# Kernel tuning notes

Measured on AMD Instinct MI355X. Metric: run time of the kernel, lower is better.

## Reference

```python
import jax, jax.numpy as jnp
import numpy as np

B, D, H, Z, E = 2048, 1024, 1024, 256, 64


def setup_inputs() -> dict:
    key = jax.random.key(0)
    ks = jax.random.split(key, 16)
    s = lambda k, shape, std=0.02: jax.random.normal(k, shape, dtype=jnp.float32) * std
    return {
        "x": jax.random.normal(ks[0], (B, D), dtype=jnp.float32),
        "h0": jax.random.normal(ks[1], (B, H), dtype=jnp.float32),
        "c0": jax.random.normal(ks[2], (B, H), dtype=jnp.float32),
        "hhat0": jax.random.normal(ks[3], (B, Z), dtype=jnp.float32),
        "chat0": jax.random.normal(ks[4], (B, Z), dtype=jnp.float32),
        "hweight": s(ks[5], (Z + H + D, 4 * Z)),
        "hbias": jnp.zeros((4 * Z,), jnp.float32),
        "zweight_h": s(ks[6], (Z, 4 * E), 0.01),
        "zweight_x": s(ks[7], (Z, 4 * E), 0.01),
        "zweight_b": s(ks[8], (Z, 4 * E), 0.01),
        "zbias_h": jnp.ones((4 * E,), jnp.float32),
        "zbias_x": jnp.ones((4 * E,), jnp.float32),
        # stacked in gate order (i, g, f, o), matching the torch cat order
        "dweight_h": jnp.full((4, E, H), 0.1 / E, jnp.float32),
        "dweight_x": jnp.full((4, E, H), 0.1 / E, jnp.float32),
        "dweight_b": s(ks[9], (4, E, H), 0.01),
        "weight": s(ks[10], (H + D, 4 * H)),
        "bias": jnp.zeros((4 * H,), jnp.float32),
    }


def reference(x, h0, c0, hhat0, chat0, hweight, hbias,
              zweight_h, zweight_x, zweight_b, zbias_h, zbias_x,
              dweight_h, dweight_x, dweight_b, weight, bias):
    # ---- hyper LSTM cell ----
    hcat = jnp.concatenate([hhat0, h0, x], axis=1)                 # [B, Z+H+D]
    hg = hcat @ hweight + hbias                                    # [B, 4Z]
    i_h, g_h, f_h, o_h = jnp.split(hg, 4, axis=1)
    chat1 = jax.nn.sigmoid(f_h) * chat0 + jax.nn.sigmoid(i_h) * jnp.tanh(g_h)
    hhat1 = jax.nn.sigmoid(o_h) * jnp.tanh(chat1)                  # [B, Z]

    # ---- embeddings z (gate order i, g, f, o) ----
    z_h = (hhat1 @ zweight_h + zbias_h).reshape(-1, 4, E)          # [B,4,E]
    z_x = (hhat1 @ zweight_x + zbias_x).reshape(-1, 4, E)
    z_b = (hhat1 @ zweight_b).reshape(-1, 4, E)

    # ---- per-gate modulation vectors d_y* : [B,4,H] -> [B,4H] ----
    d_yh = jnp.einsum('bge,geh->bgh', z_h, dweight_h).reshape(-1, 4 * H)
    d_yx = jnp.einsum('bge,geh->bgh', z_x, dweight_x).reshape(-1, 4 * H)
    d_yb = jnp.einsum('bge,geh->bgh', z_b, dweight_b).reshape(-1, 4 * H)

    # ---- main LSTM with hypernetwork modulation ----
    gates = jnp.concatenate([h0, x], axis=1) @ weight              # [B, 4H]
    gates = gates * d_yh * d_yx + d_yb + bias
    i_g, g_g, f_g, o_g = jnp.split(gates, 4, axis=1)
    c1 = jax.nn.sigmoid(f_g) * c0 + jax.nn.sigmoid(i_g) * jnp.tanh(g_g)
    h1 = jax.nn.sigmoid(o_g) * jnp.tanh(c1)
    return (h1, c1, hhat1, chat1)
```

## Files before the change

### kernel.cpp

```cpp
#include <hip/hip_runtime.h>
#include <hip/hip_bf16.h>
#include <math.h>


typedef __attribute__((ext_vector_type(8))) short bf16x8;
typedef __attribute__((ext_vector_type(4))) float f32x4;
typedef unsigned short u16;

__device__ __forceinline__ u16 f2b(float f) {
  union { float f; unsigned u; } v; v.f = f;
  unsigned r = v.u + 0x7fffu + ((v.u >> 16) & 1u);
  return (u16)(r >> 16);
}
__device__ __forceinline__ float b2f(u16 b) {
  union { unsigned u; float f; } v; v.u = ((unsigned)b) << 16; return v.f;
}
__device__ __forceinline__ float sigm(float x) {
  return __builtin_amdgcn_rcpf(1.f + __expf(-x));
}
__device__ __forceinline__ float ftanh(float x) {
  float xc = fminf(fmaxf(x, -15.f), 15.f);
  float t = __expf(2.f * xc);
  return (t - 1.f) * __builtin_amdgcn_rcpf(t + 1.f);
}
__device__ __forceinline__ float sel4(float a, float b, float c, float d, int k) {
  return (k & 2) ? ((k & 1) ? d : c) : ((k & 1) ? b : a);
}

#define GLL16(gsrc, ldst)                                                      \
  __builtin_amdgcn_global_load_lds(                                            \
      (const __attribute__((address_space(1))) void*)(gsrc),                   \
      (__attribute__((address_space(3))) void*)(ldst), 16, 0, 0)

__global__ void k_prep(const float* __restrict__ hhat0, const float* __restrict__ h0,
                       const float* __restrict__ x, const float* __restrict__ weight,
                       const float* __restrict__ hweight,
                       const float* __restrict__ zw_h, const float* __restrict__ zw_x,
                       const float* __restrict__ zw_b, const float* __restrict__ dw_h,
                       const float* __restrict__ dw_x, const float* __restrict__ dw_b,
                       u16* __restrict__ hcatb, u16* __restrict__ bt,
                       u16* __restrict__ zwT, u16* __restrict__ dwT) {
  __shared__ float tile[32][66];
  int bid = blockIdx.x;
  const int t = threadIdx.x;
  if (bid < 4608) {
    int i = bid * 256 + t;
    int b = i / 576, c4 = i % 576;
    const float* src;
    if (c4 < 64)       src = hhat0 + (long)b * 256 + c4 * 4;
    else if (c4 < 320) src = h0 + (long)b * 1024 + (c4 - 64) * 4;
    else               src = x + (long)b * 1024 + (c4 - 320) * 4;
    float4 v = *(const float4*)src;
    ushort4 o = {f2b(v.x), f2b(v.y), f2b(v.z), f2b(v.w)};
    *(ushort4*)&hcatb[(long)b * 2304 + c4 * 4] = o;
    return;
  }
  bid -= 4608;
  if (bid < 5760) {
    const int n0 = (bid % 160) * 32, k0 = (bid / 160) * 64;
    if (n0 < 4096 && k0 < 256) return;
    const int isH = (n0 >= 4096);
    const float* src; int C, sc0, sr0;
    if (isH) { src = hweight; C = 1024; sc0 = n0 - 4096; sr0 = k0; }
    else     { src = weight;  C = 4096; sc0 = n0;        sr0 = k0 - 256; }
    #pragma unroll
    for (int p = 0; p < 8; ++p) {
      int c = t & 31, r = (t >> 5) + 8 * p;
      tile[c][r] = src[(long)(sr0 + r) * C + sc0 + c];
    }
    __syncthreads();
    #pragma unroll
    for (int p = 0; p < 2; ++p) {
      int kc = t & 15, cl = (t >> 4) + 16 * p;
      int orow;
      if (isH) { int u = sc0 + cl; orow = 4096 + ((u & 255) << 2) + (u >> 8); }
      else     orow = n0 + cl;
      ushort4 o = {f2b(tile[cl][4 * kc]), f2b(tile[cl][4 * kc + 1]),
                   f2b(tile[cl][4 * kc + 2]), f2b(tile[cl][4 * kc + 3])};
      *(ushort4*)&bt[(long)orow * 2304 + k0 + 4 * kc] = o;
    }
    return;
  }
  bid -= 5760;
  const int zi = bid >> 5, bx = bid & 31;
  const float* src; u16* dst; int R, C;
  if (zi < 3) {
    src = (zi == 0) ? zw_h : (zi == 1) ? zw_x : zw_b;
    dst = zwT + (long)zi * 65536; R = 256; C = 256;
  } else {
    int s = zi - 3, tt = s >> 2, g = s & 3;
    src = ((tt == 0) ? dw_h : (tt == 1) ? dw_x : dw_b) + (long)g * 65536;
    dst = dwT + (long)s * 65536; R = 64; C = 1024;
  }
  const int nct = C / 32;
  const int c0 = (bx % nct) * 32, r0 = (bx / nct) * 64;
  #pragma unroll
  for (int p = 0; p < 8; ++p) {
    int c = t & 31, r = (t >> 5) + 8 * p;
    tile[c][r] = src[(long)(r0 + r) * C + c0 + c];
  }
  __syncthreads();
  #pragma unroll
  for (int p = 0; p < 2; ++p) {
    int kc = t & 15, cl = (t >> 4) + 16 * p;
    ushort4 o = {f2b(tile[cl][4 * kc]), f2b(tile[cl][4 * kc + 1]),
                 f2b(tile[cl][4 * kc + 2]), f2b(tile[cl][4 * kc + 3])};
    *(ushort4*)&dst[(long)(c0 + cl) * R + r0 + 4 * kc] = o;
  }
}

__global__ __launch_bounds__(512, 4)
void k_gemm_main(const u16* __restrict__ A, const u16* __restrict__ Bt,
                 const float* __restrict__ hbias, const float* __restrict__ chat0,
                 u16* __restrict__ grawb, float* __restrict__ chat1,
                 float* __restrict__ hhat1, u16* __restrict__ hhat1b) {
  constexpr int K = 2304, BK = 64;
  __shared__ __align__(16) u16 sA[2][128 * BK];
  __shared__ __align__(16) u16 sB[2][128 * BK];
  const int m0 = blockIdx.y * 128, n0 = blockIdx.x * 128;
  const int kstart = (n0 < 4096) ? 256 : 0;
  const int tid = threadIdx.x, wave = tid >> 6, lane = tid & 63;
  const int quad = lane >> 4, lrow = lane & 15;
  const int wm = (wave >> 2) * 64, wn = (wave & 3) * 32;

  const int la = tid * 16;
  const int rowa = la >> 7, qa = (((la >> 4) & 7) - rowa) & 7;
  const int lb = 8192 + tid * 16;
  const int rowb = lb >> 7, qb = (((lb >> 4) & 7) - rowb) & 7;
  const long aoff0 = ((long)(m0 + rowa) * K + qa * 8) * 2;
  const long aoff1 = ((long)(m0 + rowb) * K + qb * 8) * 2;
  const long boff0 = ((long)(n0 + rowa) * K + qa * 8) * 2;
  const long boff1 = ((long)(n0 + rowb) * K + qb * 8) * 2;

  const f32x4 vz = {0.f, 0.f, 0.f, 0.f};
  f32x4 acc[4][2];
  #pragma unroll
  for (int i = 0; i < 4; ++i)
    #pragma unroll
    for (int j = 0; j < 2; ++j) acc[i][j] = vz;

  auto stage = [&](int d, int k0) {
    const long kb = (long)k0 * 2;
    GLL16((const char*)A + aoff0 + kb, (char*)sA[d] + wave * 1024);
    GLL16((const char*)A + aoff1 + kb, (char*)sA[d] + 8192 + wave * 1024);
    GLL16((const char*)Bt + boff0 + kb, (char*)sB[d] + wave * 1024);
    GLL16((const char*)Bt + boff1 + kb, (char*)sB[d] + 8192 + wave * 1024);
  };

  auto compute = [&](int d) {
    bf16x8 af[4][2], bf[2][2];
    const char* pA = (const char*)sA[d];
    const char* pB = (const char*)sB[d];
    #pragma unroll
    for (int i = 0; i < 4; ++i) {
      int row = wm + i * 16 + lrow;
      const char* base = pA + row * 128;
      af[i][0] = *(const bf16x8*)(base + (((quad + row) & 7) << 4));
      af[i][1] = *(const bf16x8*)(base + (((4 + quad + row) & 7) << 4));
    }
    #pragma unroll
    for (int j = 0; j < 2; ++j) {
      int row = wn + j * 16 + lrow;
      const char* base = pB + row * 128;
      bf[j][0] = *(const bf16x8*)(base + (((quad + row) & 7) << 4));
      bf[j][1] = *(const bf16x8*)(base + (((4 + quad + row) & 7) << 4));
    }
    #pragma unroll
    for (int kk = 0; kk < 2; ++kk)
      #pragma unroll
      for (int i = 0; i < 4; ++i)
        #pragma unroll
        for (int j = 0; j < 2; ++j)
          acc[i][j] = __builtin_amdgcn_mfma_f32_16x16x32_bf16(af[i][kk], bf[j][kk], acc[i][j], 0, 0, 0);
  };

  const int nt = (K - kstart) >> 6;
  stage(0, kstart);
  for (int t = 0; t < nt - 1; ++t) {
    stage((t + 1) & 1, kstart + (t + 1) * BK);
    asm volatile("s_waitcnt vmcnt(4)" ::: "memory");
    __builtin_amdgcn_sched_barrier(0);
    __builtin_amdgcn_s_barrier();
    __builtin_amdgcn_sched_barrier(0);
    compute(t & 1);
    __builtin_amdgcn_s_barrier();
  }
  asm volatile("s_waitcnt vmcnt(0)" ::: "memory");
  __builtin_amdgcn_sched_barrier(0);
  __builtin_amdgcn_s_barrier();
  compute((nt - 1) & 1);

  if (n0 < 4096) {
    #pragma unroll
    for (int i = 0; i < 4; ++i)
      #pragma unroll
      for (int j = 0; j < 2; ++j)
        #pragma unroll
        for (int r = 0; r < 4; ++r) {
          int row = m0 + wm + i * 16 + quad * 4 + r;
          int col = n0 + wn + j * 16 + lrow;
          grawb[(long)row * 4096 + col] = f2b(acc[i][j][r]);
        }
  } else {
    const int ubase = (n0 - 4096) + wn;
    const int q3 = lane & 3;
    #pragma unroll
    for (int i = 0; i < 4; ++i) {
      #pragma unroll
      for (int j = 0; j < 2; ++j) {
        int u = ubase + j * 16 + lrow;
        int g = u & 3, z = u >> 2;
        float hb = hbias[g * 256 + z];
        float v0 = acc[i][j][0] + hb, v1 = acc[i][j][1] + hb;
        float v2 = acc[i][j][2] + hb, v3 = acc[i][j][3] + hb;
        float s0 = sel4(v0, v1, v2, v3, q3);
        float s1 = __shfl_xor(sel4(v0, v1, v2, v3, q3 ^ 1), 1);
        float s2 = __shfl_xor(sel4(v0, v1, v2, v3, q3 ^ 2), 2);
        float s3 = __shfl_xor(sel4(v0, v1, v2, v3, q3 ^ 3), 3);
        float vi = sel4(s0, s1, s2, s3, q3);
        float vg = sel4(s0, s1, s2, s3, q3 ^ 1);
        float vf = sel4(s0, s1, s2, s3, q3 ^ 2);
        float vo = sel4(s0, s1, s2, s3, q3 ^ 3);
        int row = m0 + wm + i * 16 + quad * 4 + q3;
        float cc = sigm(vf) * chat0[(long)row * 256 + z] + sigm(vi) * ftanh(vg);
        float hh = sigm(vo) * ftanh(cc);
        chat1[(long)row * 256 + z] = cc;
        hhat1[(long)row * 256 + z] = hh;
        hhat1b[(long)row * 256 + z] = f2b(hh);
      }
    }
  }
}

__global__ __launch_bounds__(256, 2)
void k_gemm_z(const u16* __restrict__ A, const u16* __restrict__ Bt,
              const float* __restrict__ zbh, const float* __restrict__ zbx,
              u16* __restrict__ zbout) {
  constexpr int K = 256, BK = 32;
  __shared__ __align__(16) u16 sA[64 * BK];
  __shared__ __align__(16) u16 sB[128 * BK];
  const int m0 = blockIdx.y * 64, n0 = blockIdx.x * 128;
  const int tid = threadIdx.x, wave = tid >> 6, lane = tid & 63;
  const int quad = lane >> 4, lrow = lane & 15;
  const int wm = (wave >> 1) * 32, wn = (wave & 1) * 64;

  const int sl = tid * 16;
  const int arow = sl >> 6;
  const int aq = (((sl & 63) >> 4) - (arow >> 1)) & 3;
  const long aoff = ((long)(m0 + arow) * K) * 2 + aq * 16;

  const f32x4 vz = {0.f, 0.f, 0.f, 0.f};
  f32x4 acc[2][4];
  #pragma unroll
  for (int i = 0; i < 2; ++i)
    #pragma unroll
    for (int j = 0; j < 4; ++j) acc[i][j] = vz;

  for (int k0 = 0; k0 < K; k0 += BK) {
    GLL16((const char*)A + aoff + (long)k0 * 2, (char*)sA + wave * 1024);
    #pragma unroll
    for (int c = 0; c < 2; ++c) {
      int l = c * 4096 + sl;
      int row = l >> 6;
      int q = (((l & 63) >> 4) - (row >> 1)) & 3;
      const char* g = (const char*)Bt + ((long)(n0 + row) * K + k0) * 2 + q * 16;
      GLL16(g, (char*)sB + c * 4096 + wave * 1024);
    }
    __syncthreads();
    bf16x8 af[2], bf[4];
    #pragma unroll
    for (int i = 0; i < 2; ++i) {
      int row = wm + i * 16 + lrow;
      af[i] = *(const bf16x8*)((const char*)sA + row * 64 + (((quad + (row >> 1)) & 3) << 4));
    }
    #pragma unroll
    for (int j = 0; j < 4; ++j) {
      int row = wn + j * 16 + lrow;
      bf[j] = *(const bf16x8*)((const char*)sB + row * 64 + (((quad + (row >> 1)) & 3) << 4));
    }
    #pragma unroll
    for (int i = 0; i < 2; ++i)
      #pragma unroll
      for (int j = 0; j < 4; ++j)
        acc[i][j] = __builtin_amdgcn_mfma_f32_16x16x32_bf16(af[i], bf[j], acc[i][j], 0, 0, 0);
    __syncthreads();
  }
  #pragma unroll
  for (int i = 0; i < 2; ++i) {
    #pragma unroll
    for (int j = 0; j < 4; ++j) {
      #pragma unroll
      for (int r = 0; r < 4; ++r) {
        int row = m0 + wm + i * 16 + quad * 4 + r;
        int col = n0 + wn + j * 16 + lrow;
        float v = acc[i][j][r] + ((col < 256) ? zbh[col] : (col < 512) ? zbx[col - 256] : 0.f);
        zbout[(long)row * 768 + col] = f2b(v);
      }
    }
  }
}

__global__ __launch_bounds__(256, 2)
void k_dmod_lstm(const u16* __restrict__ z, const u16* __restrict__ dwT,
                 const u16* __restrict__ grawb, const float* __restrict__ bias,
                 const float* __restrict__ c0, float* __restrict__ h1,
                 float* __restrict__ c1) {
  __shared__ __align__(16) u16 sZ[64 * 192];
  __shared__ __align__(16) u16 sW[3 * 64 * 64];
  __shared__ __align__(16) u16 sG[2][64 * 64];
  const int m0 = blockIdx.y * 64;
  const int hc0 = blockIdx.x * 64;
  const int tid = threadIdx.x, wave = tid >> 6, lane = tid & 63;
  const int quad = lane >> 4, lrow = lane & 15;
  const int wm = (wave >> 1) * 32, wn = (wave & 1) * 32;
  const f32x4 vz4 = {0.f, 0.f, 0.f, 0.f};

  f32x4 pcar[2][2];
  f32x4 ccar[2][2];

  auto stage = [&](int g) {
    #pragma unroll
    for (int c = 0; c < 6; ++c) {
      int l = c * 4096 + tid * 16;
      int ci = l >> 4, row = ci / 24, p = ci - row * 24;
      int q = p + 72 - row; q -= (q / 24) * 24;
      int tt = q >> 3, e16 = q & 7;
      const char* gz = (const char*)z + (long)(m0 + row) * 1536 + tt * 512 + g * 128 + e16 * 16;
      GLL16(gz, (char*)sZ + c * 4096 + wave * 1024);
      int t2 = l >> 13, rw = (l & 8191) >> 7, p2 = (l >> 4) & 7;
      int q2 = (p2 - rw) & 7;
      const char* gw = (const char*)dwT + (long)((t2 * 4 + g) * 1024 + hc0 + rw) * 128 + q2 * 16;
      GLL16(gw, (char*)sW + c * 4096 + wave * 1024);
    }
    #pragma unroll
    for (int c = 0; c < 2; ++c) {
      int l = c * 4096 + tid * 16;
      int row = l >> 7, off = l & 127;
      const char* gg = (const char*)grawb + ((long)(m0 + row) * 4096 + g * 1024 + hc0) * 2 + off;
      GLL16(gg, (char*)sG[g & 1] + c * 4096 + wave * 1024);
    }
  };

  stage(0);
  #pragma unroll
  for (int g = 0; g < 4; ++g) {
    __syncthreads();
    bf16x8 za2[2][3][2], wb2[2][3][2];
    #pragma unroll
    for (int kk = 0; kk < 2; ++kk) {
      #pragma unroll
      for (int t = 0; t < 3; ++t) {
        #pragma unroll
        for (int i = 0; i < 2; ++i) {
          int row = wm + i * 16 + lrow;
          int q0 = t * 8 + kk * 4 + quad;
          int ph = q0 + row; ph -= (ph / 24) * 24;
          za2[kk][t][i] = *(const bf16x8*)((const char*)sZ + row * 384 + ph * 16);
        }
        #pragma unroll
        for (int j = 0; j < 2; ++j) {
          int row = wn + j * 16 + lrow;
          int ph = ((kk * 4 + quad) + row) & 7;
          wb2[kk][t][j] = *(const bf16x8*)((const char*)sW + t * 8192 + row * 128 + ph * 16);
        }
      }
    }
    __syncthreads();
    if (g < 3) stage(g + 1);
    f32x4 aH[2][2], aX[2][2], aB[2][2];
    #pragma unroll
    for (int i = 0; i < 2; ++i)
      #pragma unroll
      for (int j = 0; j < 2; ++j) { aH[i][j] = vz4; aX[i][j] = vz4; aB[i][j] = vz4; }
    #pragma unroll
    for (int kk = 0; kk < 2; ++kk)
      #pragma unroll
      for (int i = 0; i < 2; ++i)
        #pragma unroll
        for (int j = 0; j < 2; ++j) {
          aH[i][j] = __builtin_amdgcn_mfma_f32_16x16x32_bf16(za2[kk][0][i], wb2[kk][0][j], aH[i][j], 0, 0, 0);
          aX[i][j] = __builtin_amdgcn_mfma_f32_16x16x32_bf16(za2[kk][1][i], wb2[kk][1][j], aX[i][j], 0, 0, 0);
          aB[i][j] = __builtin_amdgcn_mfma_f32_16x16x32_bf16(za2[kk][2][i], wb2[kk][2][j], aB[i][j], 0, 0, 0);
        }
    const u16* sGc = sG[g & 1];
    #pragma unroll
    for (int i = 0; i < 2; ++i) {
      #pragma unroll
      for (int j = 0; j < 2; ++j) {
        #pragma unroll
        for (int r = 0; r < 4; ++r) {
          int rowl = wm + i * 16 + quad * 4 + r;
          int col = wn + j * 16 + lrow;
          int row = m0 + rowl;
          float gr = b2f(sGc[rowl * 64 + col]);
          float v = gr * aH[i][j][r] * aX[i][j][r] + aB[i][j][r] + bias[g * 1024 + hc0 + col];
          long idx = (long)row * 1024 + hc0 + col;
          if (g == 0) pcar[i][j][r] = sigm(v);
          else if (g == 1) pcar[i][j][r] *= ftanh(v);
          else if (g == 2) {
            float cc = sigm(v) * c0[idx] + pcar[i][j][r];
            ccar[i][j][r] = cc;
            c1[idx] = cc;
          } else {
            h1[idx] = sigm(v) * ftanh(ccar[i][j][r]);
          }
        }
      }
    }
  }
}


extern "C" void kernel_launch(void* const* d_in, const int* in_sizes, int n_in,
                              void* d_out, int out_size, void* d_ws, size_t ws_size,
                              hipStream_t stream) {
  const float* x      = (const float*)d_in[0];
  const float* h0     = (const float*)d_in[1];
  const float* c0     = (const float*)d_in[2];
  const float* hhat0  = (const float*)d_in[3];
  const float* chat0  = (const float*)d_in[4];
  const float* hweight= (const float*)d_in[5];
  const float* hbias  = (const float*)d_in[6];
  const float* zw_h   = (const float*)d_in[7];
  const float* zw_x   = (const float*)d_in[8];
  const float* zw_b   = (const float*)d_in[9];
  const float* zb_h   = (const float*)d_in[10];
  const float* zb_x   = (const float*)d_in[11];
  const float* dw_h   = (const float*)d_in[12];
  const float* dw_x   = (const float*)d_in[13];
  const float* dw_b   = (const float*)d_in[14];
  const float* weight = (const float*)d_in[15];
  const float* bias   = (const float*)d_in[16];
  float* out = (float*)d_out;

  char* w = (char*)d_ws;
  auto take = [&](size_t bytes) { char* p = w; w += (bytes + 255) & ~(size_t)255; return p; };
  u16*   hcatb  = (u16*)take(2048ull * 2304 * 2);
  u16*   btc    = (u16*)take(5120ull * 2304 * 2);
  u16*   zwT    = (u16*)take(768ull * 256 * 2);
  u16*   dwT    = (u16*)take(12ull * 1024 * 64 * 2);
  u16*   grawb  = (u16*)take(2048ull * 4096 * 2);
  u16*   hhat1b = (u16*)take(2048ull * 256 * 2);
  u16*   zb16   = (u16*)take(2048ull * 768 * 2);

  float* h1_o    = out;
  float* c1_o    = out + 2048 * 1024;
  float* hhat1_o = out + 2 * 2048 * 1024;
  float* chat1_o = out + 2 * 2048 * 1024 + 2048 * 256;

  k_prep<<<4608 + 5760 + 480, 256, 0, stream>>>(
      hhat0, h0, x, weight, hweight, zw_h, zw_x, zw_b, dw_h, dw_x, dw_b,
      hcatb, btc, zwT, dwT);

  k_gemm_main<<<dim3(40, 16), 512, 0, stream>>>(hcatb, btc, hbias, chat0,
                                                grawb, chat1_o, hhat1_o, hhat1b);

  k_gemm_z<<<dim3(6, 32), 256, 0, stream>>>(hhat1b, zwT, zb_h, zb_x, zb16);

  k_dmod_lstm<<<dim3(16, 32), 256, 0, stream>>>(zb16, dwT, grawb, bias, c0, h1_o, c1_o);
}
```

Baseline: 225.4 us.

## Switch main GEMM to BK=32 with triple-buffered LDS pipeline

```diff
diff --git a/kernel.cpp b/kernel.cpp
--- a/kernel.cpp
+++ b/kernel.cpp
@@ -114,9 +114,9 @@
                  const float* __restrict__ hbias, const float* __restrict__ chat0,
                  u16* __restrict__ grawb, float* __restrict__ chat1,
                  float* __restrict__ hhat1, u16* __restrict__ hhat1b) {
-  constexpr int K = 2304, BK = 64;
-  __shared__ __align__(16) u16 sA[2][128 * BK];
-  __shared__ __align__(16) u16 sB[2][128 * BK];
+  constexpr int K = 2304, BK = 32;
+  __shared__ __align__(16) u16 sA[3][128 * BK];
+  __shared__ __align__(16) u16 sB[3][128 * BK];
   const int m0 = blockIdx.y * 128, n0 = blockIdx.x * 128;
   const int kstart = (n0 < 4096) ? 256 : 0;
   const int tid = threadIdx.x, wave = tid >> 6, lane = tid & 63;
@@ -124,13 +124,9 @@
   const int wm = (wave >> 2) * 64, wn = (wave & 3) * 32;
 
   const int la = tid * 16;
-  const int rowa = la >> 7, qa = (((la >> 4) & 7) - rowa) & 7;
-  const int lb = 8192 + tid * 16;
-  const int rowb = lb >> 7, qb = (((lb >> 4) & 7) - rowb) & 7;
-  const long aoff0 = ((long)(m0 + rowa) * K + qa * 8) * 2;
-  const long aoff1 = ((long)(m0 + rowb) * K + qb * 8) * 2;
-  const long boff0 = ((long)(n0 + rowa) * K + qa * 8) * 2;
-  const long boff1 = ((long)(n0 + rowb) * K + qb * 8) * 2;
+  const int rowa = la >> 6, qa = (((la >> 4) & 3) - rowa) & 3;
+  const long aoff = ((long)(m0 + rowa) * K + qa * 8) * 2;
+  const long boff = ((long)(n0 + rowa) * K + qa * 8) * 2;
 
   const f32x4 vz = {0.f, 0.f, 0.f, 0.f};
   f32x4 acc[4][2];
@@ -141,54 +137,51 @@
 
   auto stage = [&](int d, int k0) {
     const long kb = (long)k0 * 2;
-    GLL16((const char*)A + aoff0 + kb, (char*)sA[d] + wave * 1024);
-    GLL16((const char*)A + aoff1 + kb, (char*)sA[d] + 8192 + wave * 1024);
-    GLL16((const char*)Bt + boff0 + kb, (char*)sB[d] + wave * 1024);
-    GLL16((const char*)Bt + boff1 + kb, (char*)sB[d] + 8192 + wave * 1024);
+    GLL16((const char*)A + aoff + kb, (char*)sA[d] + wave * 1024);
+    GLL16((const char*)Bt + boff + kb, (char*)sB[d] + wave * 1024);
   };
 
   auto compute = [&](int d) {
-    bf16x8 af[4][2], bf[2][2];
+    bf16x8 af[4], bf[2];
     const char* pA = (const char*)sA[d];
     const char* pB = (const char*)sB[d];
     #pragma unroll
     for (int i = 0; i < 4; ++i) {
       int row = wm + i * 16 + lrow;
-      const char* base = pA + row * 128;
-      af[i][0] = *(const bf16x8*)(base + (((quad + row) & 7) << 4));
-      af[i][1] = *(const bf16x8*)(base + (((4 + quad + row) & 7) << 4));
+      af[i] = *(const bf16x8*)(pA + row * 64 + (((quad + row) & 3) << 4));
     }
     #pragma unroll
     for (int j = 0; j < 2; ++j) {
       int row = wn + j * 16 + lrow;
-      const char* base = pB + row * 128;
-      bf[j][0] = *(const bf16x8*)(base + (((quad + row) & 7) << 4));
-      bf[j][1] = *(const bf16x8*)(base + (((4 + quad + row) & 7) << 4));
-    }
-    #pragma unroll
-    for (int kk = 0; kk < 2; ++kk)
-      #pragma unroll
-      for (int i = 0; i < 4; ++i)
-        #pragma unroll
-        for (int j = 0; j < 2; ++j)
-          acc[i][j] = __builtin_amdgcn_mfma_f32_16x16x32_bf16(af[i][kk], bf[j][kk], acc[i][j], 0, 0, 0);
+      bf[j] = *(const bf16x8*)(pB + row * 64 + (((quad + row) & 3) << 4));
+    }
+    #pragma unroll
+    for (int i = 0; i < 4; ++i)
+      #pragma unroll
+      for (int j = 0; j < 2; ++j)
+        acc[i][j] = __builtin_amdgcn_mfma_f32_16x16x32_bf16(af[i], bf[j], acc[i][j], 0, 0, 0);
   };
 
-  const int nt = (K - kstart) >> 6;
+  const int nt = (K - kstart) >> 5;
   stage(0, kstart);
-  for (int t = 0; t < nt - 1; ++t) {
-    stage((t + 1) & 1, kstart + (t + 1) * BK);
+  stage(1, kstart + BK);
+  for (int t = 0; t < nt - 2; ++t) {
+    stage((t + 2) % 3, kstart + (t + 2) * BK);
     asm volatile("s_waitcnt vmcnt(4)" ::: "memory");
     __builtin_amdgcn_sched_barrier(0);
     __builtin_amdgcn_s_barrier();
     __builtin_amdgcn_sched_barrier(0);
-    compute(t & 1);
+    compute(t % 3);
     __builtin_amdgcn_s_barrier();
   }
+  asm volatile("s_waitcnt vmcnt(2)" ::: "memory");
+  __builtin_amdgcn_sched_barrier(0);
+  __builtin_amdgcn_s_barrier();
+  compute((nt - 2) % 3);
   asm volatile("s_waitcnt vmcnt(0)" ::: "memory");
   __builtin_amdgcn_sched_barrier(0);
   __builtin_amdgcn_s_barrier();
-  compute((nt - 1) & 1);
+  compute((nt - 1) % 3);
 
   if (n0 < 4096) {
     #pragma unroll
```

Result: no change. 223.3 us (-0.9%).
